# Kernel optimization log

Hardware: AMD Instinct MI355X
Metric: run time of the kernel (lower is better)

## Reference

```python
import jax, jax.numpy as jnp
import numpy as np

H = 4          # heads
C = 64         # per-head channels
HID = 256      # hidden_dim = H*C
L = 4          # num_layers
N = 50000      # nodes
E = 300000     # edges
G = 64         # graphs
NODE_DIMS = [80, 16, 8]
EDGE_DIMS = [8, 4]


def setup_inputs() -> dict:
    key = jax.random.key(0)
    ks = iter(jax.random.split(key, 64))
    def nrm(shape, fan_in):
        return jax.random.normal(next(ks), shape, dtype=jnp.float32) * (1.0 / np.sqrt(fan_in))
    inp = {}
    inp['x'] = jax.random.randint(next(ks), (N, 3), 0, 8)
    inp['edge_attr'] = jax.random.randint(next(ks), (E, 2), 0, 4)
    inp['edge_index'] = jax.random.randint(next(ks), (2, E), 0, N)
    inp['batch'] = jnp.sort(jax.random.randint(next(ks), (N,), 0, G))
    inp['scalars'] = jax.random.uniform(next(ks), (G, 5), dtype=jnp.float32)
    inp['num_graphs'] = G
    # categorical embedding tables (summed per field)
    inp['node_emb0'] = nrm((NODE_DIMS[0], HID), HID)
    inp['node_emb1'] = nrm((NODE_DIMS[1], HID), HID)
    inp['node_emb2'] = nrm((NODE_DIMS[2], HID), HID)
    inp['edge_emb0'] = nrm((EDGE_DIMS[0], HID), HID)
    inp['edge_emb1'] = nrm((EDGE_DIMS[1], HID), HID)
    # stacked per-layer TransformerConv params
    inp['Wq'] = nrm((L, HID, HID), HID); inp['bq'] = jnp.zeros((L, HID))
    inp['Wk'] = nrm((L, HID, HID), HID); inp['bk'] = jnp.zeros((L, HID))
    inp['Wv'] = nrm((L, HID, HID), HID); inp['bv'] = jnp.zeros((L, HID))
    inp['We'] = nrm((L, HID, HID), HID); inp['be'] = jnp.zeros((L, HID))
    inp['Wskip'] = nrm((L, HID, HID), HID); inp['bskip'] = jnp.zeros((L, HID))
    inp['Wbeta'] = nrm((L, 3 * HID, 1), 3 * HID)  # beta gate, bias=False in PyG
    inp['ln_g'] = jnp.ones((L, HID)); inp['ln_b'] = jnp.zeros((L, HID))
    # pragma scalar encoder
    inp['pw1'] = nrm((5, HID), 5); inp['pb1'] = jnp.zeros((HID,))
    inp['pw2'] = nrm((HID, HID), HID); inp['pb2'] = jnp.zeros((HID,))
    # readout MLP
    inp['rw1'] = nrm((HID, HID), HID); inp['rb1'] = jnp.zeros((HID,))
    inp['rw2'] = nrm((HID, HID // 2), HID); inp['rb2'] = jnp.zeros((HID // 2,))
    inp['rw3'] = nrm((HID // 2, 4), HID // 2); inp['rb3'] = jnp.zeros((4,))
    return inp


def _forward(scalars, node_emb0, node_emb1, node_emb2, edge_emb0, edge_emb1,
             Wq, bq, Wk, bk, Wv, bv, We, be, Wskip, bskip, Wbeta, ln_g, ln_b,
             pw1, pb1, pw2, pb2, rw1, rb1, rw2, rb2, rw3, rb3,
             x, edge_attr, edge_index, batch, num_graphs):
    n = x.shape[0]
    src, dst = edge_index[0], edge_index[1]
    # CategoricalEmbedding: sum of per-field embeddings
    h = node_emb0[x[:, 0]] + node_emb1[x[:, 1]] + node_emb2[x[:, 2]]      # [N, HID]
    ef = edge_emb0[edge_attr[:, 0]] + edge_emb1[edge_attr[:, 1]]          # [E, HID]
    scale = 1.0 / jnp.sqrt(jnp.asarray(C, h.dtype))
    for l in range(L):
        q = (h @ Wq[l] + bq[l]).reshape(n, H, C)
        kN = (h @ Wk[l] + bk[l]).reshape(n, H, C)
        vN = (h @ Wv[l] + bv[l]).reshape(n, H, C)
        e = (ef @ We[l] + be[l]).reshape(-1, H, C)                        # [E, H, C]
        kj = kN[src] + e                                                  # edge feat added to keys
        alpha = jnp.sum(q[dst] * kj, axis=-1) * scale                     # [E, H]
        # segment softmax over incoming edges per destination node
        amax = jax.ops.segment_max(alpha, dst, num_segments=n)
        amax = jnp.where(jnp.isfinite(amax), amax, 0.0)
        ea = jnp.exp(alpha - amax[dst])
        denom = jax.ops.segment_sum(ea, dst, num_segments=n)
        attn = ea / jnp.maximum(denom, 1e-16)[dst]                        # [E, H]
        msg = (vN[src] + e) * attn[..., None]                             # edge feat added to values
        out = jax.ops.segment_sum(msg, dst, num_segments=n).reshape(n, HID)
        # beta gated skip (TransformerConv beta=True, root_weight=True)
        r = h @ Wskip[l] + bskip[l]
        beta = jax.nn.sigmoid(jnp.concatenate([out, r, out - r], axis=-1) @ Wbeta[l])  # [N,1]
        out = beta * r + (1.0 - beta) * out
        out = jax.nn.relu(out)
        # LayerNorm over hidden dim
        mu = jnp.mean(out, axis=-1, keepdims=True)
        var = jnp.var(out, axis=-1, keepdims=True)
        out = (out - mu) * jax.lax.rsqrt(var + 1e-5) * ln_g[l] + ln_b[l]
        h = h + out                                                       # residual (dropout off in eval)
    pooled = jax.ops.segment_sum(h, batch, num_segments=num_graphs)       # global_add_pool
    p = jax.nn.relu(scalars @ pw1 + pb1) @ pw2 + pb2                      # pragma encoder
    pooled = pooled + p
    z = jax.nn.relu(pooled @ rw1 + rb1)
    z = jax.nn.relu(z @ rw2 + rb2)
    return z @ rw3 + rb3                                                  # [G, 4]


def reference(x, edge_attr, edge_index, batch, scalars, num_graphs,
              node_emb0, node_emb1, node_emb2, edge_emb0, edge_emb1,
              Wq, bq, Wk, bk, Wv, bv, We, be, Wskip, bskip, Wbeta, ln_g, ln_b,
              pw1, pb1, pw2, pb2, rw1, rb1, rw2, rb2, rw3, rb3):
    return _forward(scalars, node_emb0, node_emb1, node_emb2, edge_emb0, edge_emb1,
                    Wq, bq, Wk, bk, Wv, bv, We, be, Wskip, bskip, Wbeta, ln_g, ln_b,
                    pw1, pb1, pw2, pb2, rw1, rb1, rw2, rb2, rw3, rb3,
                    x, edge_attr, edge_index, batch, num_graphs)
```

## Files before the change

kernel.cpp:

```cpp
#include <hip/hip_runtime.h>
#include <hip/hip_bf16.h>

typedef short short8 __attribute__((ext_vector_type(8)));
typedef float floatx4 __attribute__((ext_vector_type(4)));
typedef __hip_bfloat16 bf16;

#define HID 256
#define NL  4
#define AS1 __attribute__((address_space(1)))
#define AS3 __attribute__((address_space(3)))

__device__ __forceinline__ float b2f(bf16 v) { return __bfloat162float(v); }
__device__ __forceinline__ bf16 f2b(float v) { return __float2bfloat16(v); }
__device__ __forceinline__ float us2f(unsigned short u) {
    unsigned int x = ((unsigned int)u) << 16;
    return __uint_as_float(x);
}
__device__ __forceinline__ unsigned short f2us(float v) {
    bf16 t = __float2bfloat16(v);
    return *reinterpret_cast<unsigned short*>(&t);
}

template <int CTRL>
__device__ __forceinline__ float row_ror_add(float x) {
    return x + __int_as_float(__builtin_amdgcn_update_dpp(
        0, __float_as_int(x), CTRL, 0xF, 0xF, true));
}

__global__ void zero_ws_kernel(int* __restrict__ a, int* __restrict__ b, int n,
                               float* __restrict__ p, int np) {
    int i = blockIdx.x * 256 + threadIdx.x;
    if (i < n) { a[i] = 0; b[i] = 0; }
    if (i < np) p[i] = 0.f;
}

__global__ __launch_bounds__(256) void node_embed_kernel(const int* __restrict__ x,
                                  const float* __restrict__ e0, const float* __restrict__ e1,
                                  const float* __restrict__ e2,
                                  bf16* __restrict__ hbf, int N) {
    const int tid = threadIdx.x;
    const int n = blockIdx.x * 4 + (tid >> 6);
    if (n >= N) return;
    const int c4 = (tid & 63) * 4;
    const int i0 = x[n * 3], i1 = x[n * 3 + 1], i2 = x[n * 3 + 2];
    const float4 a = *reinterpret_cast<const float4*>(e0 + i0 * HID + c4);
    const float4 b = *reinterpret_cast<const float4*>(e1 + i1 * HID + c4);
    const float4 c = *reinterpret_cast<const float4*>(e2 + i2 * HID + c4);
    ushort4 o;
    o.x = f2us(a.x + b.x + c.x);
    o.y = f2us(a.y + b.y + c.y);
    o.z = f2us(a.z + b.z + c.z);
    o.w = f2us(a.w + b.w + c.w);
    *reinterpret_cast<ushort4*>(hbf + (size_t)n * HID + c4) = o;
}

__global__ void ecombo_embed_kernel(const float* __restrict__ e0, const float* __restrict__ e1,
                                    float* __restrict__ ec) {
    int i = blockIdx.x, c = threadIdx.x;
    ec[i * HID + c] = e0[(i >> 2) * HID + c] + e1[(i & 3) * HID + c];
}

__global__ void edge_prep_kernel(const int* __restrict__ ea, const int* __restrict__ dst,
                                 int E, int* __restrict__ ecid, int* __restrict__ counts) {
    int e = blockIdx.x * 256 + threadIdx.x;
    if (e < E) {
        ecid[e] = ea[e * 2] * 4 + ea[e * 2 + 1];
        atomicAdd(&counts[dst[e]], 1);
    }
}

__global__ void combo_proj_kernel(const float* __restrict__ ec, const float* __restrict__ We,
                                  const float* __restrict__ be, float* __restrict__ ecp4) {
    __shared__ float row[HID];
    int l = blockIdx.x >> 5, i = blockIdx.x & 31, c = threadIdx.x;
    row[c] = ec[i * HID + c];
    __syncthreads();
    const float* We_l = We + (size_t)l * 65536;
    float a = be[l * 256 + c];
    for (int k = 0; k < HID; ++k) a += row[k] * We_l[k * HID + c];
    ecp4[(size_t)l * 32 * HID + i * HID + c] = a;
}

__global__ void scan_local_kernel(const int* __restrict__ counts, int N,
                                  int* __restrict__ incl, int* __restrict__ bsum) {
    __shared__ int sd[256];
    int i = threadIdx.x;
    int idx = blockIdx.x * 256 + i;
    sd[i] = (idx < N) ? counts[idx] : 0;
    __syncthreads();
    for (int off = 1; off < 256; off <<= 1) {
        int t = (i >= off) ? sd[i - off] : 0;
        __syncthreads();
        sd[i] += t;
        __syncthreads();
    }
    if (idx < N) incl[idx] = sd[i];
    if (i == 255) bsum[blockIdx.x] = sd[255];
}

__global__ void scan_block_kernel(const int* __restrict__ bsum, int nb, int* __restrict__ boff) {
    __shared__ int sd[256];
    int i = threadIdx.x;
    sd[i] = (i < nb) ? bsum[i] : 0;
    __syncthreads();
    for (int off = 1; off < 256; off <<= 1) {
        int t = (i >= off) ? sd[i - off] : 0;
        __syncthreads();
        sd[i] += t;
        __syncthreads();
    }
    if (i < nb) boff[i] = (i == 0) ? 0 : sd[i - 1];
}

__global__ void scan_add_kernel(const int* __restrict__ incl, const int* __restrict__ boff,
                                int N, int* __restrict__ indptr) {
    int idx = blockIdx.x * 256 + threadIdx.x;
    if (idx < N) indptr[idx + 1] = incl[idx] + boff[blockIdx.x];
    if (idx == 0) indptr[0] = 0;
}

__global__ void fill_sorted_kernel(const int* __restrict__ dst, const int* __restrict__ srcv,
                                   const int* __restrict__ ecid, const int* __restrict__ indptr,
                                   int E, int* __restrict__ fill, int2* __restrict__ sorted2) {
    int e = blockIdx.x * 256 + threadIdx.x;
    if (e < E) {
        int d = dst[e];
        int pos = indptr[d] + atomicAdd(&fill[d], 1);
        sorted2[pos] = make_int2(srcv[e] << 11, ecid[e] << 10);
    }
    if (e < 4) sorted2[E + e] = make_int2(0, 0);
}

__global__ __launch_bounds__(256) void pack_wcat_kernel(
    const float* __restrict__ Wq, const float* __restrict__ Wk,
    const float* __restrict__ Wv, const float* __restrict__ Ws,
    bf16* __restrict__ wcatT) {
    __shared__ bf16 tile[64][65];
    const int jt = blockIdx.x;
    const int kt = blockIdx.y;
    const int l  = blockIdx.z;
    const int tid = threadIdx.x;
    const int jl = tid & 63;
    const int j = jt * 64 + jl;
    const float* W;
    int jj;
    if (j < 256)      { W = Wq; jj = j; }
    else if (j < 512) { W = Ws; jj = j - 256; }
    else {
        int g = (j - 512) >> 3, r = (j - 512) & 7;
        if (r < 4) { W = Wk; jj = 4 * g + r; }
        else       { W = Wv; jj = 4 * g + r - 4; }
    }
    const float* Wbase = W + (size_t)l * 65536 + jj + (size_t)(kt * 64) * 256;
    const int kr = tid >> 6;
#pragma unroll
    for (int i = 0; i < 16; ++i) {
        const int kl = kr + i * 4;
        tile[kl][jl] = f2b(Wbase[(size_t)kl * 256]);
    }
    __syncthreads();
    const int kl2 = tid & 63;
    const int jr = tid >> 6;
    bf16* out = wcatT + (size_t)l * 262144 + (size_t)(jt * 64) * 256 + kt * 64 + kl2;
#pragma unroll
    for (int i = 0; i < 16; ++i) {
        const int jl2 = jr + i * 4;
        out[(size_t)jl2 * 256] = tile[kl2][jl2];
    }
}

__global__ void pack_bias_kernel(const float* __restrict__ bq, const float* __restrict__ bk,
                                 const float* __restrict__ bv, const float* __restrict__ bs,
                                 float* __restrict__ bcat) {
    int idx = blockIdx.x * 256 + threadIdx.x;
    if (idx < 4096) {
        int l = idx >> 10, j = idx & 1023;
        const float* B;
        int jj;
        if (j < 256)      { B = bq; jj = j; }
        else if (j < 512) { B = bs; jj = j - 256; }
        else {
            int g = (j - 512) >> 3, r = (j - 512) & 7;
            if (r < 4) { B = bk; jj = 4 * g + r; }
            else       { B = bv; jj = 4 * g + r - 4; }
        }
        bcat[idx] = B[l * 256 + jj];
    }
}

__global__ __launch_bounds__(256, 4) void gemm_stream_kernel(
    const bf16* __restrict__ A, const bf16* __restrict__ BT,
    const float* __restrict__ bias, bf16* __restrict__ C, int M) {
    __shared__ __align__(16) bf16 sW[64 * 256];
    __shared__ __align__(16) bf16 sC[2][4][1152];
    const int tid = threadIdx.x;
    const int lane = tid & 63;
    const int wave = tid >> 6;
    const int d = blockIdx.x;
    const int id = (d & 7) * 196 + (d >> 3);
    const int n0 = (id & 15) * 64;
    const int y  = id >> 4;
    const int fr = lane & 15;
    const int quad = lane >> 4;
    const int wsw = fr & 7;

    {
        const char* wsrc = (const char*)(BT + (size_t)n0 * 256);
#pragma unroll
        for (int r = 0; r < 8; ++r) {
            const int g = r * 256 + wave * 64 + lane;
            const int sg = g ^ ((g >> 5) & 7);
            __builtin_amdgcn_global_load_lds(
                (const AS1 void*)(wsrc + (size_t)sg * 16),
                (AS3 void*)(sW + (r * 256 + wave * 64) * 8), 16, 0, 0);
        }
    }
    float bias4[4];
#pragma unroll
    for (int ni = 0; ni < 4; ++ni) bias4[ni] = bias[n0 + ni * 16 + fr];
    __syncthreads();

    const int row16 = lane >> 3;
    const int c16 = lane & 7;

    for (int ms = y; ms * 256 < M; ms += 98) {
        const int mrow = ms * 256 + wave * 64;
        floatx4 acc[4][4] = {};
        const bf16* ap[4];
#pragma unroll
        for (int mi = 0; mi < 4; ++mi)
            ap[mi] = A + (size_t)min(mrow + mi * 16 + fr, M - 1) * 256 + quad * 8;
#pragma unroll
        for (int kk = 0; kk < 8; ++kk) {
            const int go = (((kk << 2) | quad) ^ wsw) * 8;
            short8 bfm[4];
#pragma unroll
            for (int ni = 0; ni < 4; ++ni)
                bfm[ni] = *reinterpret_cast<const short8*>(sW + (ni * 16 + fr) * 256 + go);
            short8 af[4];
#pragma unroll
            for (int mi = 0; mi < 4; ++mi)
                af[mi] = *reinterpret_cast<const short8*>(ap[mi] + kk * 32);
#pragma unroll
            for (int mi = 0; mi < 4; ++mi)
#pragma unroll
                for (int ni = 0; ni < 4; ++ni)
                    acc[mi][ni] = __builtin_amdgcn_mfma_f32_16x16x32_bf16(af[mi], bfm[ni], acc[mi][ni], 0, 0, 0);
        }
#pragma unroll
        for (int mi = 0; mi < 4; ++mi) {
            bf16* wb = &sC[mi & 1][wave][0];
#pragma unroll
            for (int ni = 0; ni < 4; ++ni)
#pragma unroll
                for (int r = 0; r < 4; ++r)
                    wb[(quad * 4 + r) * 72 + ni * 16 + fr] = f2b(acc[mi][ni][r] + bias4[ni]);
#pragma unroll
            for (int h = 0; h < 2; ++h) {
                const int rr = row16 + h * 8;
                const int grow = mrow + mi * 16 + rr;
                const uint4 vv = *reinterpret_cast<const uint4*>(wb + rr * 72 + c16 * 8);
                if (grow < M)
                    *reinterpret_cast<uint4*>(C + (size_t)grow * 1024 + n0 + c16 * 8) = vv;
            }
        }
    }
}

__global__ __launch_bounds__(256) void attn_node_kernel(
    const bf16* __restrict__ qkvs,
    const float* __restrict__ ecp,
    const int* __restrict__ indptr, const int2* __restrict__ sorted2,
    const float* __restrict__ Wbeta_l, const float* __restrict__ lng, const float* __restrict__ lnb,
    bf16* __restrict__ hbf, int N) {
    const int tid = threadIdx.x;
    const int wv = tid >> 6;
    const int lane = tid & 63;
    const int n = blockIdx.x * 4 + wv;
    if (n >= N) return;
    const int c0 = lane * 4;
    const ushort4 qu = *reinterpret_cast<const ushort4*>(qkvs + (size_t)n * 1024 + c0);
    const float q0 = us2f(qu.x), q1 = us2f(qu.y), q2 = us2f(qu.z), q3 = us2f(qu.w);
    float a0 = 0.f, a1 = 0.f, a2 = 0.f, a3 = 0.f, wsum = 0.f;
    const int e0 = indptr[n], e1 = indptr[n + 1];
    const char* __restrict__ kvb = (const char*)qkvs + 1024 + lane * 16;
    const char* __restrict__ epb = (const char*)ecp + c0 * 4;

    auto edge_body = [&](const uint4& kv, const float4& ep) {
        const float k0 = us2f((unsigned short)(kv.x & 0xffff)), k1 = us2f((unsigned short)(kv.x >> 16));
        const float k2 = us2f((unsigned short)(kv.y & 0xffff)), k3 = us2f((unsigned short)(kv.y >> 16));
        const float v0 = us2f((unsigned short)(kv.z & 0xffff)), v1 = us2f((unsigned short)(kv.z >> 16));
        const float v2 = us2f((unsigned short)(kv.w & 0xffff)), v3 = us2f((unsigned short)(kv.w >> 16));
        float t = q0 * (k0 + ep.x) + q1 * (k1 + ep.y) + q2 * (k2 + ep.z) + q3 * (k3 + ep.w);
        t = row_ror_add<0x121>(t);
        t = row_ror_add<0x122>(t);
        t = row_ror_add<0x124>(t);
        t = row_ror_add<0x128>(t);
        const float w = __expf(t * 0.125f);
        a0 += w * (v0 + ep.x);
        a1 += w * (v1 + ep.y);
        a2 += w * (v2 + ep.z);
        a3 += w * (v3 + ep.w);
        wsum += w;
    };

    if (e0 < e1) {
        int2 m0 = sorted2[e0];
        int2 m1 = sorted2[e0 + 1];
        uint4 kv0 = *reinterpret_cast<const uint4*>(kvb + (unsigned)m0.x);
        uint4 kv1 = *reinterpret_cast<const uint4*>(kvb + (unsigned)m1.x);
        int ee = e0;
        for (; ee + 1 < e1; ee += 2) {
            const int2 mN0 = sorted2[ee + 2];
            const int2 mN1 = sorted2[ee + 3];
            const uint4 kvN0 = *reinterpret_cast<const uint4*>(kvb + (unsigned)mN0.x);
            const uint4 kvN1 = *reinterpret_cast<const uint4*>(kvb + (unsigned)mN1.x);
            const float4 ep0 = *reinterpret_cast<const float4*>(epb + (unsigned)m0.y);
            const float4 ep1 = *reinterpret_cast<const float4*>(epb + (unsigned)m1.y);
            edge_body(kv0, ep0);
            edge_body(kv1, ep1);
            m0 = mN0; m1 = mN1;
            kv0 = kvN0; kv1 = kvN1;
        }
        if (ee < e1) {
            const float4 ep0 = *reinterpret_cast<const float4*>(epb + (unsigned)m0.y);
            edge_body(kv0, ep0);
        }
    }
    const float inv = (wsum > 0.f) ? 1.f / wsum : 0.f;
    const float o0 = a0 * inv, o1 = a1 * inv, o2 = a2 * inv, o3 = a3 * inv;
    const ushort4 ru = *reinterpret_cast<const ushort4*>(qkvs + (size_t)n * 1024 + 256 + c0);
    const float r0 = us2f(ru.x), r1 = us2f(ru.y), r2 = us2f(ru.z), r3 = us2f(ru.w);
    const float4 w1 = *reinterpret_cast<const float4*>(Wbeta_l + c0);
    const float4 w2 = *reinterpret_cast<const float4*>(Wbeta_l + 256 + c0);
    const float4 w3 = *reinterpret_cast<const float4*>(Wbeta_l + 512 + c0);
    float tb = o0 * w1.x + o1 * w1.y + o2 * w1.z + o3 * w1.w
             + r0 * w2.x + r1 * w2.y + r2 * w2.z + r3 * w2.w
             + (o0 - r0) * w3.x + (o1 - r1) * w3.y + (o2 - r2) * w3.z + (o3 - r3) * w3.w;
#pragma unroll
    for (int off = 32; off > 0; off >>= 1) tb += __shfl_xor(tb, off);
    const float beta = 1.f / (1.f + __expf(-tb));
    float g0 = fmaxf(beta * r0 + (1.f - beta) * o0, 0.f);
    float g1 = fmaxf(beta * r1 + (1.f - beta) * o1, 0.f);
    float g2 = fmaxf(beta * r2 + (1.f - beta) * o2, 0.f);
    float g3 = fmaxf(beta * r3 + (1.f - beta) * o3, 0.f);
    float s1 = g0 + g1 + g2 + g3;
    float s2 = g0 * g0 + g1 * g1 + g2 * g2 + g3 * g3;
#pragma unroll
    for (int off = 32; off > 0; off >>= 1) { s1 += __shfl_xor(s1, off); s2 += __shfl_xor(s2, off); }
    const float mu = s1 * (1.f / 256.f);
    const float var = s2 * (1.f / 256.f) - mu * mu;
    const float rish = rsqrtf(fmaxf(var, 0.f) + 1e-5f);
    const float4 gg = *reinterpret_cast<const float4*>(lng + c0);
    const float4 bb = *reinterpret_cast<const float4*>(lnb + c0);
    ushort4 hb = *reinterpret_cast<ushort4*>(hbf + (size_t)n * HID + c0);
    float h0 = us2f(hb.x) + (g0 - mu) * rish * gg.x + bb.x;
    float h1 = us2f(hb.y) + (g1 - mu) * rish * gg.y + bb.y;
    float h2 = us2f(hb.z) + (g2 - mu) * rish * gg.z + bb.z;
    float h3 = us2f(hb.w) + (g3 - mu) * rish * gg.w + bb.w;
    hb.x = f2us(h0); hb.y = f2us(h1); hb.z = f2us(h2); hb.w = f2us(h3);
    *reinterpret_cast<ushort4*>(hbf + (size_t)n * HID + c0) = hb;
}

__global__ __launch_bounds__(256) void pool_kernel(const bf16* __restrict__ hbf,
                                                   const int* __restrict__ batch,
                                                   float* __restrict__ pooled, int N) {
    __shared__ int sb[64];
    const int c = threadIdx.x;
    const int n0 = blockIdx.x * 64;
    const int cnt = min(64, N - n0);
    if (c < 64 && c < cnt) sb[c] = batch[n0 + c];
    __syncthreads();
    float acc = 0.f;
    int gcur = sb[0];
    for (int i = 0; i < cnt; ++i) {
        const int g = sb[i];
        if (g != gcur) {
            atomicAdd(&pooled[(size_t)gcur * HID + c], acc);
            acc = 0.f;
            gcur = g;
        }
        acc += b2f(hbf[(size_t)(n0 + i) * HID + c]);
    }
    atomicAdd(&pooled[(size_t)gcur * HID + c], acc);
}

__global__ void pragma_kernel(const float* __restrict__ scalars,
                              const float* __restrict__ pw1, const float* __restrict__ pb1,
                              const float* __restrict__ pw2, const float* __restrict__ pb2,
                              float* __restrict__ pooled) {
    int g = blockIdx.x, c = threadIdx.x;
    __shared__ float s5[5];
    __shared__ float t1[256];
    if (c < 5) s5[c] = scalars[g * 5 + c];
    __syncthreads();
    float a = pb1[c];
    for (int k = 0; k < 5; ++k) a += s5[k] * pw1[k * 256 + c];
    t1[c] = fmaxf(a, 0.f);
    __syncthreads();
    float p = pb2[c];
    for (int j = 0; j < 256; ++j) p += t1[j] * pw2[j * 256 + c];
    pooled[g * 256 + c] += p;
}

__global__ void readout_kernel(const float* __restrict__ pooled,
                               const float* __restrict__ rw1, const float* __restrict__ rb1,
                               const float* __restrict__ rw2, const float* __restrict__ rb2,
                               const float* __restrict__ rw3, const float* __restrict__ rb3,
                               float* __restrict__ out) {
    int g = blockIdx.x, c = threadIdx.x;
    __shared__ float pl[256], z1[256], z2[128];
    pl[c] = pooled[g * 256 + c];
    __syncthreads();
    float z = rb1[c];
    for (int k = 0; k < 256; ++k) z += pl[k] * rw1[k * 256 + c];
    z1[c] = fmaxf(z, 0.f);
    __syncthreads();
    if (c < 128) {
        float v = rb2[c];
        for (int j = 0; j < 256; ++j) v += z1[j] * rw2[j * 128 + c];
        z2[c] = fmaxf(v, 0.f);
    }
    __syncthreads();
    if (c < 4) {
        float o = rb3[c];
        for (int j = 0; j < 128; ++j) o += z2[j] * rw3[j * 4 + c];
        out[g * 4 + c] = o;
    }
}

extern "C" void kernel_launch(void* const* d_in, const int* in_sizes, int n_in,
                              void* d_out, int out_size, void* d_ws, size_t ws_size,
                              hipStream_t stream) {
    const int* x          = (const int*)d_in[0];
    const int* edge_attr  = (const int*)d_in[1];
    const int* edge_index = (const int*)d_in[2];
    const int* batch      = (const int*)d_in[3];
    const float* scalars  = (const float*)d_in[4];
    const float* ne0 = (const float*)d_in[6];
    const float* ne1 = (const float*)d_in[7];
    const float* ne2 = (const float*)d_in[8];
    const float* ee0 = (const float*)d_in[9];
    const float* ee1 = (const float*)d_in[10];
    const float* Wq = (const float*)d_in[11];
    const float* bq = (const float*)d_in[12];
    const float* Wk = (const float*)d_in[13];
    const float* bk = (const float*)d_in[14];
    const float* Wv = (const float*)d_in[15];
    const float* bv = (const float*)d_in[16];
    const float* We = (const float*)d_in[17];
    const float* be = (const float*)d_in[18];
    const float* Wskip = (const float*)d_in[19];
    const float* bskip = (const float*)d_in[20];
    const float* Wbeta = (const float*)d_in[21];
    const float* ln_g = (const float*)d_in[22];
    const float* ln_b = (const float*)d_in[23];
    const float* pw1 = (const float*)d_in[24];
    const float* pb1 = (const float*)d_in[25];
    const float* pw2 = (const float*)d_in[26];
    const float* pb2 = (const float*)d_in[27];
    const float* rw1 = (const float*)d_in[28];
    const float* rb1 = (const float*)d_in[29];
    const float* rw2 = (const float*)d_in[30];
    const float* rb2 = (const float*)d_in[31];
    const float* rw3 = (const float*)d_in[32];
    const float* rb3 = (const float*)d_in[33];

    const int N = in_sizes[0] / 3;
    const int E = in_sizes[1] / 2;
    const int G = in_sizes[4] / 5;

    char* base = (char*)d_ws;
    size_t off = 0;
    auto carve = [&](size_t bytes) -> char* {
        char* p = base + off;
        off += (bytes + 255) & ~(size_t)255;
        return p;
    };
    bf16*  hbf    = (bf16*)carve((size_t)N * HID * 2);
    bf16*  qkvs   = (bf16*)carve((size_t)N * 1024 * 2);
    float* ec     = (float*)carve((size_t)32 * HID * 4);
    float* ecp4   = (float*)carve((size_t)NL * 32 * HID * 4);
    int*   ecid   = (int*)carve((size_t)E * 4);
    float* pooled = (float*)carve((size_t)G * HID * 4);
    bf16*  wcatT  = (bf16*)carve((size_t)NL * 1024 * 256 * 2);
    float* bcat   = (float*)carve((size_t)NL * 1024 * 4);
    int* counts   = (int*)carve((size_t)N * 4);
    int* fill     = (int*)carve((size_t)N * 4);
    int* incl     = (int*)carve((size_t)N * 4);
    int* bsum     = (int*)carve(4096);
    int* boff     = (int*)carve(4096);
    int* indptr   = (int*)carve((size_t)(N + 1) * 4);
    int2* sorted2 = (int2*)carve((size_t)(E + 4) * 8);

    const int* srcv = edge_index;
    const int* dstv = edge_index + E;

    zero_ws_kernel<<<(N + 255) / 256, 256, 0, stream>>>(counts, fill, N, pooled, G * HID);
    node_embed_kernel<<<(N + 3) / 4, 256, 0, stream>>>(x, ne0, ne1, ne2, hbf, N);
    ecombo_embed_kernel<<<32, 256, 0, stream>>>(ee0, ee1, ec);
    edge_prep_kernel<<<(E + 255) / 256, 256, 0, stream>>>(edge_attr, dstv, E, ecid, counts);
    {
        dim3 gp(16, 4, 4);
        pack_wcat_kernel<<<gp, 256, 0, stream>>>(Wq, Wk, Wv, Wskip, wcatT);
    }
    pack_bias_kernel<<<16, 256, 0, stream>>>(bq, bk, bv, bskip, bcat);
    combo_proj_kernel<<<NL * 32, 256, 0, stream>>>(ec, We, be, ecp4);

    int nsb = (N + 255) / 256;
    scan_local_kernel<<<nsb, 256, 0, stream>>>(counts, N, incl, bsum);
    scan_block_kernel<<<1, 256, 0, stream>>>(bsum, nsb, boff);
    scan_add_kernel<<<nsb, 256, 0, stream>>>(incl, boff, N, indptr);
    fill_sorted_kernel<<<(E + 255) / 256, 256, 0, stream>>>(dstv, srcv, ecid, indptr, E, fill, sorted2);

    for (int l = 0; l < NL; ++l) {
        gemm_stream_kernel<<<1568, 256, 0, stream>>>(hbf, wcatT + (size_t)l * 262144,
                                                     bcat + (size_t)l * 1024, qkvs, N);
        attn_node_kernel<<<(N + 3) / 4, 256, 0, stream>>>(qkvs, ecp4 + (size_t)l * 32 * HID,
                                                          indptr, sorted2,
                                                          Wbeta + (size_t)l * 768,
                                                          ln_g + (size_t)l * 256, ln_b + (size_t)l * 256,
                                                          hbf, N);
    }

    pool_kernel<<<(N + 63) / 64, 256, 0, stream>>>(hbf, batch, pooled, N);
    pragma_kernel<<<G, 256, 0, stream>>>(scalars, pw1, pb1, pw2, pb2, pooled);
    readout_kernel<<<G, 256, 0, stream>>>(pooled, rw1, rb1, rw2, rb2, rw3, rb3, (float*)d_out);
}
```

Before: 714.0 us.

## Store K/V projections as FP8 to halve gathered bytes in attention

```diff
diff --git a/kernel.cpp b/kernel.cpp
--- a/kernel.cpp
+++ b/kernel.cpp
@@ -3,10 +3,12 @@
 
 typedef short short8 __attribute__((ext_vector_type(8)));
 typedef float floatx4 __attribute__((ext_vector_type(4)));
+typedef float floatx2 __attribute__((ext_vector_type(2)));
 typedef __hip_bfloat16 bf16;
 
 #define HID 256
 #define NL  4
+#define QROW 1536
 #define AS1 __attribute__((address_space(1)))
 #define AS3 __attribute__((address_space(3)))
 
@@ -126,7 +128,7 @@
     if (e < E) {
         int d = dst[e];
         int pos = indptr[d] + atomicAdd(&fill[d], 1);
-        sorted2[pos] = make_int2(srcv[e] << 11, ecid[e] << 10);
+        sorted2[pos] = make_int2(srcv[e] * QROW, ecid[e] << 10);
     }
     if (e < 4) sorted2[E + e] = make_int2(0, 0);
 }
@@ -190,9 +192,9 @@
 
 __global__ __launch_bounds__(256, 4) void gemm_stream_kernel(
     const bf16* __restrict__ A, const bf16* __restrict__ BT,
-    const float* __restrict__ bias, bf16* __restrict__ C, int M) {
+    const float* __restrict__ bias, char* __restrict__ Cb, int M) {
     __shared__ __align__(16) bf16 sW[64 * 256];
-    __shared__ __align__(16) bf16 sC[2][4][1152];
+    __shared__ __align__(16) bf16 sC[4][1024];
     const int tid = threadIdx.x;
     const int lane = tid & 63;
     const int wave = tid >> 6;
@@ -247,28 +249,48 @@
                 for (int ni = 0; ni < 4; ++ni)
                     acc[mi][ni] = __builtin_amdgcn_mfma_f32_16x16x32_bf16(af[mi], bfm[ni], acc[mi][ni], 0, 0, 0);
         }
+        bf16* wb = &sC[wave][0];
 #pragma unroll
         for (int mi = 0; mi < 4; ++mi) {
-            bf16* wb = &sC[mi & 1][wave][0];
 #pragma unroll
             for (int ni = 0; ni < 4; ++ni)
 #pragma unroll
                 for (int r = 0; r < 4; ++r)
-                    wb[(quad * 4 + r) * 72 + ni * 16 + fr] = f2b(acc[mi][ni][r] + bias4[ni]);
+                    wb[(quad * 4 + r) * 64 + (((ni * 2 + (fr >> 3)) ^ (quad << 1)) << 3) + (fr & 7)] =
+                        f2b(acc[mi][ni][r] + bias4[ni]);
 #pragma unroll
             for (int h = 0; h < 2; ++h) {
                 const int rr = row16 + h * 8;
+                const int pg = c16 ^ (((rr >> 2) & 3) << 1);
+                const uint4 vv = *reinterpret_cast<const uint4*>(wb + rr * 64 + (pg << 3));
                 const int grow = mrow + mi * 16 + rr;
-                const uint4 vv = *reinterpret_cast<const uint4*>(wb + rr * 72 + c16 * 8);
-                if (grow < M)
-                    *reinterpret_cast<uint4*>(C + (size_t)grow * 1024 + n0 + c16 * 8) = vv;
+                if (grow < M) {
+                    char* crow = Cb + (size_t)grow * QROW;
+                    if (n0 < 512) {
+                        *reinterpret_cast<uint4*>(crow + n0 * 2 + c16 * 16) = vv;
+                    } else {
+                        const float f0 = us2f((unsigned short)(vv.x & 0xffff)), f1 = us2f((unsigned short)(vv.x >> 16));
+                        const float f2 = us2f((unsigned short)(vv.y & 0xffff)), f3 = us2f((unsigned short)(vv.y >> 16));
+                        const float f4 = us2f((unsigned short)(vv.z & 0xffff)), f5 = us2f((unsigned short)(vv.z >> 16));
+                        const float f6 = us2f((unsigned short)(vv.w & 0xffff)), f7 = us2f((unsigned short)(vv.w >> 16));
+                        int lo = 0, hi = 0;
+                        lo = __builtin_amdgcn_cvt_pk_fp8_f32(f0, f1, lo, false);
+                        lo = __builtin_amdgcn_cvt_pk_fp8_f32(f2, f3, lo, true);
+                        hi = __builtin_amdgcn_cvt_pk_fp8_f32(f4, f5, hi, false);
+                        hi = __builtin_amdgcn_cvt_pk_fp8_f32(f6, f7, hi, true);
+                        uint2 o;
+                        o.x = (unsigned)lo;
+                        o.y = (unsigned)hi;
+                        *reinterpret_cast<uint2*>(crow + 1024 + (n0 - 512) + c16 * 8) = o;
+                    }
+                }
             }
         }
     }
 }
 
 __global__ __launch_bounds__(256) void attn_node_kernel(
-    const bf16* __restrict__ qkvs,
+    const char* __restrict__ qkvs,
     const float* __restrict__ ecp,
     const int* __restrict__ indptr, const int2* __restrict__ sorted2,
     const float* __restrict__ Wbeta_l, const float* __restrict__ lng, const float* __restrict__ lnb,
@@ -279,42 +301,42 @@
     const int n = blockIdx.x * 4 + wv;
     if (n >= N) return;
     const int c0 = lane * 4;
-    const ushort4 qu = *reinterpret_cast<const ushort4*>(qkvs + (size_t)n * 1024 + c0);
+    const ushort4 qu = *reinterpret_cast<const ushort4*>(qkvs + (size_t)n * QROW + lane * 8);
     const float q0 = us2f(qu.x), q1 = us2f(qu.y), q2 = us2f(qu.z), q3 = us2f(qu.w);
     float a0 = 0.f, a1 = 0.f, a2 = 0.f, a3 = 0.f, wsum = 0.f;
     const int e0 = indptr[n], e1 = indptr[n + 1];
-    const char* __restrict__ kvb = (const char*)qkvs + 1024 + lane * 16;
+    const char* __restrict__ kvb = qkvs + 1024 + lane * 8;
     const char* __restrict__ epb = (const char*)ecp + c0 * 4;
 
-    auto edge_body = [&](const uint4& kv, const float4& ep) {
-        const float k0 = us2f((unsigned short)(kv.x & 0xffff)), k1 = us2f((unsigned short)(kv.x >> 16));
-        const float k2 = us2f((unsigned short)(kv.y & 0xffff)), k3 = us2f((unsigned short)(kv.y >> 16));
-        const float v0 = us2f((unsigned short)(kv.z & 0xffff)), v1 = us2f((unsigned short)(kv.z >> 16));
-        const float v2 = us2f((unsigned short)(kv.w & 0xffff)), v3 = us2f((unsigned short)(kv.w >> 16));
-        float t = q0 * (k0 + ep.x) + q1 * (k1 + ep.y) + q2 * (k2 + ep.z) + q3 * (k3 + ep.w);
+    auto edge_body = [&](const uint2& kv, const float4& ep) {
+        const floatx2 ka = __builtin_amdgcn_cvt_pk_f32_fp8(kv.x, false);
+        const floatx2 kb = __builtin_amdgcn_cvt_pk_f32_fp8(kv.x, true);
+        const floatx2 va = __builtin_amdgcn_cvt_pk_f32_fp8(kv.y, false);
+        const floatx2 vb = __builtin_amdgcn_cvt_pk_f32_fp8(kv.y, true);
+        float t = q0 * (ka.x + ep.x) + q1 * (ka.y + ep.y) + q2 * (kb.x + ep.z) + q3 * (kb.y + ep.w);
         t = row_ror_add<0x121>(t);
         t = row_ror_add<0x122>(t);
         t = row_ror_add<0x124>(t);
         t = row_ror_add<0x128>(t);
         const float w = __expf(t * 0.125f);
-        a0 += w * (v0 + ep.x);
-        a1 += w * (v1 + ep.y);
-        a2 += w * (v2 + ep.z);
-        a3 += w * (v3 + ep.w);
+        a0 += w * (va.x + ep.x);
+        a1 += w * (va.y + ep.y);
+        a2 += w * (vb.x + ep.z);
+        a3 += w * (vb.y + ep.w);
         wsum += w;
     };
 
     if (e0 < e1) {
         int2 m0 = sorted2[e0];
         int2 m1 = sorted2[e0 + 1];
-        uint4 kv0 = *reinterpret_cast<const uint4*>(kvb + (unsigned)m0.x);
-        uint4 kv1 = *reinterpret_cast<const uint4*>(kvb + (unsigned)m1.x);
+        uint2 kv0 = *reinterpret_cast<const uint2*>(kvb + (unsigned)m0.x);
+        uint2 kv1 = *reinterpret_cast<const uint2*>(kvb + (unsigned)m1.x);
         int ee = e0;
         for (; ee + 1 < e1; ee += 2) {
             const int2 mN0 = sorted2[ee + 2];
             const int2 mN1 = sorted2[ee + 3];
-            const uint4 kvN0 = *reinterpret_cast<const uint4*>(kvb + (unsigned)mN0.x);
-            const uint4 kvN1 = *reinterpret_cast<const uint4*>(kvb + (unsigned)mN1.x);
+            const uint2 kvN0 = *reinterpret_cast<const uint2*>(kvb + (unsigned)mN0.x);
+            const uint2 kvN1 = *reinterpret_cast<const uint2*>(kvb + (unsigned)mN1.x);
             const float4 ep0 = *reinterpret_cast<const float4*>(epb + (unsigned)m0.y);
             const float4 ep1 = *reinterpret_cast<const float4*>(epb + (unsigned)m1.y);
             edge_body(kv0, ep0);
@@ -329,7 +351,7 @@
     }
     const float inv = (wsum > 0.f) ? 1.f / wsum : 0.f;
     const float o0 = a0 * inv, o1 = a1 * inv, o2 = a2 * inv, o3 = a3 * inv;
-    const ushort4 ru = *reinterpret_cast<const ushort4*>(qkvs + (size_t)n * 1024 + 256 + c0);
+    const ushort4 ru = *reinterpret_cast<const ushort4*>(qkvs + (size_t)n * QROW + 512 + lane * 8);
     const float r0 = us2f(ru.x), r1 = us2f(ru.y), r2 = us2f(ru.z), r3 = us2f(ru.w);
     const float4 w1 = *reinterpret_cast<const float4*>(Wbeta_l + c0);
     const float4 w2 = *reinterpret_cast<const float4*>(Wbeta_l + 256 + c0);
@@ -478,7 +500,7 @@
         return p;
     };
     bf16*  hbf    = (bf16*)carve((size_t)N * HID * 2);
-    bf16*  qkvs   = (bf16*)carve((size_t)N * 1024 * 2);
+    char*  qkvs   = (char*)carve((size_t)N * QROW);
     float* ec     = (float*)carve((size_t)32 * HID * 4);
     float* ecp4   = (float*)carve((size_t)NL * 32 * HID * 4);
     int*   ecid   = (int*)carve((size_t)E * 4);
```

After: 704.8 us. About the same (-1.3%).

## Replace LDS-staged streaming GEMM with register-resident weight tiles per block

Applied to the files above, without the earlier changes.

```diff
diff --git a/kernel.cpp b/kernel.cpp
--- a/kernel.cpp
+++ b/kernel.cpp
@@ -188,81 +188,72 @@
     }
 }
 
-__global__ __launch_bounds__(256, 4) void gemm_stream_kernel(
+__global__ __launch_bounds__(256, 2) void gemm_reg_kernel(
     const bf16* __restrict__ A, const bf16* __restrict__ BT,
     const float* __restrict__ bias, bf16* __restrict__ C, int M) {
-    __shared__ __align__(16) bf16 sW[64 * 256];
-    __shared__ __align__(16) bf16 sC[2][4][1152];
+    __shared__ __align__(16) bf16 sC[2][4][1024];
     const int tid = threadIdx.x;
     const int lane = tid & 63;
     const int wave = tid >> 6;
     const int d = blockIdx.x;
-    const int id = (d & 7) * 196 + (d >> 3);
-    const int n0 = (id & 15) * 64;
-    const int y  = id >> 4;
+    const int id = (d & 7) * 784 + (d >> 3);
+    const int cg = id & 3;
+    const int mrow = (id >> 2) * 32;
+    const int n0 = cg * 256 + wave * 64;
     const int fr = lane & 15;
     const int quad = lane >> 4;
-    const int wsw = fr & 7;
-
-    {
-        const char* wsrc = (const char*)(BT + (size_t)n0 * 256);
-#pragma unroll
-        for (int r = 0; r < 8; ++r) {
-            const int g = r * 256 + wave * 64 + lane;
-            const int sg = g ^ ((g >> 5) & 7);
-            __builtin_amdgcn_global_load_lds(
-                (const AS1 void*)(wsrc + (size_t)sg * 16),
-                (AS3 void*)(sW + (r * 256 + wave * 64) * 8), 16, 0, 0);
-        }
-    }
+
+    short8 bq[4][8];
+#pragma unroll
+    for (int ni = 0; ni < 4; ++ni)
+#pragma unroll
+        for (int kk = 0; kk < 8; ++kk)
+            bq[ni][kk] = *reinterpret_cast<const short8*>(
+                BT + (size_t)(n0 + ni * 16 + fr) * 256 + kk * 32 + quad * 8);
     float bias4[4];
 #pragma unroll
     for (int ni = 0; ni < 4; ++ni) bias4[ni] = bias[n0 + ni * 16 + fr];
-    __syncthreads();
+
+    const bf16* ap0 = A + (size_t)min(mrow + fr, M - 1) * 256 + quad * 8;
+    const bf16* ap1 = A + (size_t)min(mrow + 16 + fr, M - 1) * 256 + quad * 8;
+
+    floatx4 acc[2][4] = {};
+    short8 a0 = *reinterpret_cast<const short8*>(ap0);
+    short8 a1 = *reinterpret_cast<const short8*>(ap1);
+#pragma unroll
+    for (int kk = 0; kk < 8; ++kk) {
+        short8 an = a0, bn = a1;
+        if (kk < 7) {
+            an = *reinterpret_cast<const short8*>(ap0 + (kk + 1) * 32);
+            bn = *reinterpret_cast<const short8*>(ap1 + (kk + 1) * 32);
+        }
+#pragma unroll
+        for (int ni = 0; ni < 4; ++ni) {
+            acc[0][ni] = __builtin_amdgcn_mfma_f32_16x16x32_bf16(a0, bq[ni][kk], acc[0][ni], 0, 0, 0);
+            acc[1][ni] = __builtin_amdgcn_mfma_f32_16x16x32_bf16(a1, bq[ni][kk], acc[1][ni], 0, 0, 0);
+        }
+        a0 = an; a1 = bn;
+    }
 
     const int row16 = lane >> 3;
     const int c16 = lane & 7;
-
-    for (int ms = y; ms * 256 < M; ms += 98) {
-        const int mrow = ms * 256 + wave * 64;
-        floatx4 acc[4][4] = {};
-        const bf16* ap[4];
-#pragma unroll
-        for (int mi = 0; mi < 4; ++mi)
-            ap[mi] = A + (size_t)min(mrow + mi * 16 + fr, M - 1) * 256 + quad * 8;
-#pragma unroll
-        for (int kk = 0; kk < 8; ++kk) {
-            const int go = (((kk << 2) | quad) ^ wsw) * 8;
-            short8 bfm[4];
-#pragma unroll
-            for (int ni = 0; ni < 4; ++ni)
-                bfm[ni] = *reinterpret_cast<const short8*>(sW + (ni * 16 + fr) * 256 + go);
-            short8 af[4];
-#pragma unroll
-            for (int mi = 0; mi < 4; ++mi)
-                af[mi] = *reinterpret_cast<const short8*>(ap[mi] + kk * 32);
-#pragma unroll
-            for (int mi = 0; mi < 4; ++mi)
-#pragma unroll
-                for (int ni = 0; ni < 4; ++ni)
-                    acc[mi][ni] = __builtin_amdgcn_mfma_f32_16x16x32_bf16(af[mi], bfm[ni], acc[mi][ni], 0, 0, 0);
-        }
-#pragma unroll
-        for (int mi = 0; mi < 4; ++mi) {
-            bf16* wb = &sC[mi & 1][wave][0];
-#pragma unroll
-            for (int ni = 0; ni < 4; ++ni)
-#pragma unroll
-                for (int r = 0; r < 4; ++r)
-                    wb[(quad * 4 + r) * 72 + ni * 16 + fr] = f2b(acc[mi][ni][r] + bias4[ni]);
-#pragma unroll
-            for (int h = 0; h < 2; ++h) {
-                const int rr = row16 + h * 8;
-                const int grow = mrow + mi * 16 + rr;
-                const uint4 vv = *reinterpret_cast<const uint4*>(wb + rr * 72 + c16 * 8);
-                if (grow < M)
-                    *reinterpret_cast<uint4*>(C + (size_t)grow * 1024 + n0 + c16 * 8) = vv;
-            }
+#pragma unroll
+    for (int mi = 0; mi < 2; ++mi) {
+        bf16* wb = &sC[mi][wave][0];
+#pragma unroll
+        for (int ni = 0; ni < 4; ++ni)
+#pragma unroll
+            for (int r = 0; r < 4; ++r)
+                wb[(quad * 4 + r) * 64 + (((ni * 2 + (fr >> 3)) ^ (quad << 1)) << 3) + (fr & 7)] =
+                    f2b(acc[mi][ni][r] + bias4[ni]);
+#pragma unroll
+        for (int h = 0; h < 2; ++h) {
+            const int rr = row16 + h * 8;
+            const int pg = c16 ^ (((rr >> 2) & 3) << 1);
+            const uint4 vv = *reinterpret_cast<const uint4*>(wb + rr * 64 + (pg << 3));
+            const int grow = mrow + mi * 16 + rr;
+            if (grow < M)
+                *reinterpret_cast<uint4*>(C + (size_t)grow * 1024 + n0 + c16 * 8) = vv;
         }
     }
 }
@@ -514,8 +505,8 @@
     fill_sorted_kernel<<<(E + 255) / 256, 256, 0, stream>>>(dstv, srcv, ecid, indptr, E, fill, sorted2);
 
     for (int l = 0; l < NL; ++l) {
-        gemm_stream_kernel<<<1568, 256, 0, stream>>>(hbf, wcatT + (size_t)l * 262144,
-                                                     bcat + (size_t)l * 1024, qkvs, N);
+        gemm_reg_kernel<<<6272, 256, 0, stream>>>(hbf, wcatT + (size_t)l * 262144,
+                                                  bcat + (size_t)l * 1024, qkvs, N);
         attn_node_kernel<<<(N + 3) / 4, 256, 0, stream>>>(qkvs, ecp4 + (size_t)l * 32 * HID,
                                                           indptr, sorted2,
                                                           Wbeta + (size_t)l * 768,
```

New measurement: 0.9998 ms. 40.0% more time.
